# Optimization experiments

Measured on AMD Instinct MI355X. Metric: run time of the kernel, lower is better.

## Reference

```python
import jax, jax.numpy as jnp
import numpy as np

NUM_QUANTIZERS = 8  # num_quantizes in __init__


def l2norm(t, eps=1e-12):
    return t / jnp.clip(jnp.linalg.norm(t, axis=-1, keepdims=True), eps)


def setup_inputs() -> dict:
    key = jax.random.key(0)
    k1, k2 = jax.random.split(key)
    x = jax.random.normal(k1, (1, 16384, 512), dtype=jnp.float32)
    codebook = jax.random.normal(k2, (2048, 512), dtype=jnp.float32)
    return {"x": x, "codebook": codebook}


def reference(x, codebook):
    # cosine-sim codebook: codes live on the unit sphere
    cb = l2norm(codebook)  # [K, D]

    def step(residual, _):
        rn = l2norm(residual)                       # [1, S, D]
        sim = jnp.einsum('bsd,kd->bsk', rn, cb)     # [1, S, K]
        idx = jnp.argmax(sim, axis=-1)              # [1, S]
        q = cb[idx]                                 # [1, S, D] gather
        # commit loss: mse(quantize.detach(), input)
        commit = jnp.mean((jax.lax.stop_gradient(q) - residual) ** 2)
        # straight-through estimator
        q_st = residual + jax.lax.stop_gradient(q - residual)
        return residual - q_st, (q_st, idx, commit)

    _, (quantized, indices, commits) = jax.lax.scan(
        step, x, None, length=NUM_QUANTIZERS)
    # quantized: [n, 1, S, D]; sum over quantizer axis (keepdim batch=1)
    quantized_sum = jnp.sum(quantized, axis=0)      # [1, S, D]
    all_indices = jnp.transpose(indices, (1, 2, 0))  # [1, S, n]
    commit_losses = commits[None, :]                # [1, n]
    return quantized_sum, all_indices, commit_losses
```

## Files before the change

### kernel.cpp

```cpp
#include <hip/hip_runtime.h>
#include <math.h>


#define TOKENS 16384
#define DDIM   512
#define NCODE  2048
#define NQ     8
#define CHUNK  4096
#define DTHR   1e-3f

typedef short   bf16x8  __attribute__((ext_vector_type(8)));
typedef float   f32x4   __attribute__((ext_vector_type(4)));
typedef short   s16x8   __attribute__((ext_vector_type(8)));

#define GLOBAL_AS __attribute__((address_space(1)))
#define LDS_AS    __attribute__((address_space(3)))

#define CBN_OFF  0u
#define G_OFF    1048576u
#define S_OFF    5242880u
#define XHI_OFF  13631488u
#define XLO_OFF  17825792u
#define BHI_OFF  22020096u
#define BLO_OFF  22544384u
#define ACC_OFF  23068672u

#define QS_OFF   0u
#define IDX_OFF  8388608u
#define CL_OFF   8519680u

__device__ inline unsigned short f2bf(float f) {
  unsigned u = __float_as_uint(f);
  return (unsigned short)((u + 0x7FFFu + ((u >> 16) & 1u)) >> 16);
}
__device__ inline float bf2f(unsigned short h) {
  return __uint_as_float(((unsigned)h) << 16);
}

__global__ __launch_bounds__(256) void normalize_cb(const float* __restrict__ cb,
                                                    float* __restrict__ cbn,
                                                    short* __restrict__ bhi,
                                                    short* __restrict__ blo,
                                                    float* __restrict__ acc) {
  if (blockIdx.x == 0 && threadIdx.x < NQ) acc[threadIdx.x] = 0.0f;
  int lane = threadIdx.x & 63;
  int wv   = threadIdx.x >> 6;
  int row  = blockIdx.x * 4 + wv;
  const float4* rp = (const float4*)(cb + (size_t)row * DDIM);
  float4 a = rp[lane * 2 + 0];
  float4 b = rp[lane * 2 + 1];
  float ss = a.x*a.x + a.y*a.y + a.z*a.z + a.w*a.w
           + b.x*b.x + b.y*b.y + b.z*b.z + b.w*b.w;
  #pragma unroll
  for (int o = 1; o < 64; o <<= 1) ss += __shfl_xor(ss, o);
  float nrm = fmaxf(sqrtf(ss), 1e-12f);
  float v[8] = {a.x/nrm, a.y/nrm, a.z/nrm, a.w/nrm,
                b.x/nrm, b.y/nrm, b.z/nrm, b.w/nrm};
  float4* op = (float4*)(cbn + (size_t)row * DDIM);
  op[lane*2+0] = make_float4(v[0], v[1], v[2], v[3]);
  op[lane*2+1] = make_float4(v[4], v[5], v[6], v[7]);

  s16x8 h8, l8;
  #pragma unroll
  for (int i = 0; i < 8; ++i) {
    unsigned short h = f2bf(v[i]);
    h8[i] = (short)h;
    l8[i] = (short)f2bf(v[i] - bf2f(h));
  }
  int nb = row >> 7, rr = row & 127, ks = lane >> 2, g = lane & 3;
  size_t gidx = ((size_t)((nb * 16 + ks) * 4 + g) * 128 + rr) * 8;
  *(s16x8*)(bhi + gidx) = h8;
  *(s16x8*)(blo + gidx) = l8;
}

__global__ __launch_bounds__(256) void split_x(const float* __restrict__ x,
                                               short* __restrict__ xhi,
                                               short* __restrict__ xlo) {
  int gid = blockIdx.x * 256 + threadIdx.x;
  int r  = gid & 127;
  int g  = (gid >> 7) & 3;
  int ks = (gid >> 9) & 15;
  int mb = gid >> 13;
  const float4* src = (const float4*)(x + (size_t)(mb * 128 + r) * DDIM + ks * 32 + g * 8);
  float4 v0 = src[0], v1 = src[1];
  float v[8] = {v0.x, v0.y, v0.z, v0.w, v1.x, v1.y, v1.z, v1.w};
  s16x8 h8, l8;
  #pragma unroll
  for (int i = 0; i < 8; ++i) {
    unsigned short h = f2bf(v[i]);
    h8[i] = (short)h;
    l8[i] = (short)f2bf(v[i] - bf2f(h));
  }
  *(s16x8*)(xhi + (size_t)gid * 8) = h8;
  *(s16x8*)(xlo + (size_t)gid * 8) = l8;
}

__global__ void finalize(const float* __restrict__ acc, float* __restrict__ out) {
  if (threadIdx.x < NQ)
    out[CL_OFF + threadIdx.x] = acc[threadIdx.x] * (1.0f / ((float)TOKENS * (float)DDIM));
}

__global__ __launch_bounds__(256) void gemm_nt(const float* __restrict__ A,
                                               const float* __restrict__ B,
                                               float* __restrict__ C) {
  const int K = DDIM, N = NCODE;
  __shared__ float As[2][16][132];
  __shared__ float Bs[2][16][132];
  const int bn = blockIdx.x * 128;
  const int bm = blockIdx.y * 128;
  const int t  = threadIdx.x;
  const int tx = t & 15;
  const int ty = t >> 4;
  const int lr = t >> 2;
  const int lc = (t & 3) * 4;

  float acc[8][8];
  #pragma unroll
  for (int i = 0; i < 8; ++i)
    #pragma unroll
    for (int j = 0; j < 8; ++j) acc[i][j] = 0.0f;

  const float* Ap = A + (size_t)(bm + lr) * K + lc;
  const float* Bp = B + (size_t)(bn + lr) * K + lc;

  float4 a0 = *(const float4*)(Ap);
  float4 a1 = *(const float4*)(Ap + (size_t)64 * K);
  float4 b0 = *(const float4*)(Bp);
  float4 b1 = *(const float4*)(Bp + (size_t)64 * K);

  int cur = 0;
  for (int k0 = 0; k0 < K; k0 += 16) {
    As[cur][lc+0][lr]    = a0.x; As[cur][lc+1][lr]    = a0.y;
    As[cur][lc+2][lr]    = a0.z; As[cur][lc+3][lr]    = a0.w;
    As[cur][lc+0][lr+64] = a1.x; As[cur][lc+1][lr+64] = a1.y;
    As[cur][lc+2][lr+64] = a1.z; As[cur][lc+3][lr+64] = a1.w;
    Bs[cur][lc+0][lr]    = b0.x; Bs[cur][lc+1][lr]    = b0.y;
    Bs[cur][lc+2][lr]    = b0.z; Bs[cur][lc+3][lr]    = b0.w;
    Bs[cur][lc+0][lr+64] = b1.x; Bs[cur][lc+1][lr+64] = b1.y;
    Bs[cur][lc+2][lr+64] = b1.z; Bs[cur][lc+3][lr+64] = b1.w;
    if (k0 + 16 < K) {
      a0 = *(const float4*)(Ap + k0 + 16);
      a1 = *(const float4*)(Ap + (size_t)64 * K + k0 + 16);
      b0 = *(const float4*)(Bp + k0 + 16);
      b1 = *(const float4*)(Bp + (size_t)64 * K + k0 + 16);
    }
    __syncthreads();
    #pragma unroll
    for (int kk = 0; kk < 16; ++kk) {
      float av[8], bv[8];
      *(float4*)(av + 0) = *(const float4*)&As[cur][kk][ty * 4];
      *(float4*)(av + 4) = *(const float4*)&As[cur][kk][ty * 4 + 64];
      *(float4*)(bv + 0) = *(const float4*)&Bs[cur][kk][tx * 4];
      *(float4*)(bv + 4) = *(const float4*)&Bs[cur][kk][tx * 4 + 64];
      #pragma unroll
      for (int i = 0; i < 8; ++i)
        #pragma unroll
        for (int j = 0; j < 8; ++j) acc[i][j] += av[i] * bv[j];
    }
    cur ^= 1;
  }

  #pragma unroll
  for (int i = 0; i < 8; ++i) {
    int m = bm + ty * 4 + (i & 3) + ((i >> 2) << 6);
    float4 v0 = make_float4(acc[i][0], acc[i][1], acc[i][2], acc[i][3]);
    float4 v1 = make_float4(acc[i][4], acc[i][5], acc[i][6], acc[i][7]);
    *(float4*)&C[(size_t)m * N + bn + tx * 4]      = v0;
    *(float4*)&C[(size_t)m * N + bn + tx * 4 + 64] = v1;
  }
}

__global__ __launch_bounds__(256) void mfma_s(const short* __restrict__ xhi,
                                              const short* __restrict__ xlo,
                                              const short* __restrict__ bhi,
                                              const short* __restrict__ blo,
                                              float* __restrict__ S, int mb0) {
  __shared__ short lds[2][4][4096];
  const int l  = threadIdx.x & 63;
  const int w  = threadIdx.x >> 6;
  const int wm = w >> 1, wn = w & 1;
  const int MB = mb0 + blockIdx.y;
  const int NB = blockIdx.x;

  const short* src = (w == 0) ? xhi : (w == 1) ? xlo : (w == 2) ? bhi : blo;
  const size_t tb  = (size_t)(((w < 2 ? MB : NB) * 16)) * 4096;

  f32x4 acc[4][4];
  #pragma unroll
  for (int i = 0; i < 4; ++i)
    #pragma unroll
    for (int j = 0; j < 4; ++j)
      acc[i][j] = (f32x4){0.f, 0.f, 0.f, 0.f};

  #define STAGE(buf, ks)                                                        \
    {                                                                           \
      const short* gsrc = src + tb + (size_t)(ks) * 4096 + l * 8;               \
      short* ldst = &lds[buf][w][0];                                            \
      _Pragma("unroll")                                                         \
      for (int c = 0; c < 8; ++c)                                               \
        __builtin_amdgcn_global_load_lds(                                       \
            (GLOBAL_AS const unsigned int*)(gsrc + c * 512),                    \
            (LDS_AS unsigned int*)(ldst + c * 512), 16, 0, 0);                  \
    }

  STAGE(0, 0);
  const int g = l >> 4, c16 = l & 15;
  for (int ks = 0; ks < 16; ++ks) {
    const int cur = ks & 1;
    __syncthreads();
    if (ks < 15) STAGE(cur ^ 1, ks + 1);
    bf16x8 ah[4], al[4], bh[4], bl[4];
    #pragma unroll
    for (int f = 0; f < 4; ++f) {
      int ar = (g * 128 + (wm * 64 + f * 16 + c16)) * 8;
      int br = (g * 128 + (wn * 64 + f * 16 + c16)) * 8;
      ah[f] = *(const bf16x8*)&lds[cur][0][ar];
      al[f] = *(const bf16x8*)&lds[cur][1][ar];
      bh[f] = *(const bf16x8*)&lds[cur][2][br];
      bl[f] = *(const bf16x8*)&lds[cur][3][br];
    }
    #pragma unroll
    for (int fm = 0; fm < 4; ++fm)
      #pragma unroll
      for (int fn = 0; fn < 4; ++fn) {
        acc[fm][fn] = __builtin_amdgcn_mfma_f32_16x16x32_bf16(ah[fm], bh[fn], acc[fm][fn], 0, 0, 0);
        acc[fm][fn] = __builtin_amdgcn_mfma_f32_16x16x32_bf16(ah[fm], bl[fn], acc[fm][fn], 0, 0, 0);
        acc[fm][fn] = __builtin_amdgcn_mfma_f32_16x16x32_bf16(al[fm], bh[fn], acc[fm][fn], 0, 0, 0);
      }
  }
  #undef STAGE

  #pragma unroll
  for (int fm = 0; fm < 4; ++fm)
    #pragma unroll
    for (int fn = 0; fn < 4; ++fn)
      #pragma unroll
      for (int reg = 0; reg < 4; ++reg) {
        int m = blockIdx.y * 128 + wm * 64 + fm * 16 + g * 4 + reg;
        int n = NB * 128 + wn * 64 + fn * 16 + c16;
        S[(size_t)m * NCODE + n] = acc[fm][fn][reg];
      }
}

__global__ __launch_bounds__(256) void vq_steps(const float* __restrict__ S,
                                                const float* __restrict__ G,
                                                const float* __restrict__ cbn,
                                                const float* __restrict__ x,
                                                float* __restrict__ out,
                                                float* __restrict__ acc,
                                                int tok0) {
  const int lane = threadIdx.x & 63;
  const int wv   = threadIdx.x >> 6;
  const int trel = blockIdx.x * 4 + wv;
  const int tok  = tok0 + trel;

  float s[32];
  const float4* sp = (const float4*)(S + (size_t)trel * NCODE);
  #pragma unroll
  for (int q = 0; q < 8; ++q) {
    float4 v = sp[q * 64 + lane];
    s[q*4+0] = v.x; s[q*4+1] = v.y; s[q*4+2] = v.z; s[q*4+3] = v.w;
  }

  const float4* xp = (const float4*)(x + (size_t)tok * DDIM);
  float4 x0 = xp[lane * 2 + 0];
  float4 x1 = xp[lane * 2 + 1];
  float rho = x0.x*x0.x + x0.y*x0.y + x0.z*x0.z + x0.w*x0.w
            + x1.x*x1.x + x1.y*x1.y + x1.z*x1.z + x1.w*x1.w;
  #pragma unroll
  for (int o = 1; o < 64; o <<= 1) rho += __shfl_xor(rho, o);

  float qs[8] = {0.f,0.f,0.f,0.f,0.f,0.f,0.f,0.f};
  __shared__ float cl[4][NQ];
  int i0=0,i1=0,i2=0,i3=0,i4=0,i5=0,i6=0;

  for (int t = 0; t < NQ; ++t) {
    float tv[16]; int tc[16];
    #pragma unroll
    for (int r = 0; r < 16; ++r) {
      int ca = ((2*r) >> 2 << 8) + lane * 4 + ((2*r) & 3);
      float va = s[2*r], vb = s[2*r+1];
      bool b = vb > va;
      tv[r] = b ? vb : va;
      tc[r] = b ? ca + 1 : ca;
    }
    #pragma unroll
    for (int h = 8; h >= 1; h >>= 1) {
      #pragma unroll
      for (int r = 0; r < 16; ++r) {
        if (r < h) {
          bool b = tv[r + h] > tv[r];
          tv[r] = b ? tv[r + h] : tv[r];
          tc[r] = b ? tc[r + h] : tc[r];
        }
      }
    }
    float mv = tv[0];
    int   mc = tc[0];
    #pragma unroll
    for (int o = 1; o < 64; o <<= 1) {
      float ov = __shfl_xor(mv, o);
      int   oc = __shfl_xor(mc, o);
      if (ov > mv || (ov == mv && oc < mc)) { mv = ov; mc = oc; }
    }

    int cloc = 0;
    #pragma unroll
    for (int r = 0; r < 32; ++r) cloc += (s[r] >= mv - DTHR) ? 1 : 0;
    #pragma unroll
    for (int o = 1; o < 64; o <<= 1) cloc += __shfl_xor(cloc, o);
    if (cloc > 1) {
      float bv = -3.4e38f; int bc = 0x7FFFFFFF; int seen = 0;
      for (int r = 0; r < 32 && seen < 64; ++r) {
        unsigned long long mask = __ballot(s[r] >= mv - DTHR);
        while (mask && seen < 64) {
          int L = __ffsll((unsigned long long)mask) - 1;
          mask &= mask - 1;
          int kc = ((r >> 2) << 8) + L * 4 + (r & 3);
          if (lane == seen) {
            float e = 0.f;
            const float* xr = x + (size_t)tok * DDIM;
            const float* cr = cbn + (size_t)kc * DDIM;
            for (int k = 0; k < DDIM; ++k) e = fmaf(xr[k], cr[k], e);
            if (t > 0) e -= G[(size_t)i0 * NCODE + kc];
            if (t > 1) e -= G[(size_t)i1 * NCODE + kc];
            if (t > 2) e -= G[(size_t)i2 * NCODE + kc];
            if (t > 3) e -= G[(size_t)i3 * NCODE + kc];
            if (t > 4) e -= G[(size_t)i4 * NCODE + kc];
            if (t > 5) e -= G[(size_t)i5 * NCODE + kc];
            if (t > 6) e -= G[(size_t)i6 * NCODE + kc];
            bv = e; bc = kc;
          }
          ++seen;
        }
      }
      #pragma unroll
      for (int o = 1; o < 64; o <<= 1) {
        float ov = __shfl_xor(bv, o);
        int   oc = __shfl_xor(bc, o);
        if (ov > bv || (ov == bv && oc < bc)) { bv = ov; bc = oc; }
      }
      mv = bv; mc = bc;
    }

    if (t == 0) i0 = mc; else if (t == 1) i1 = mc; else if (t == 2) i2 = mc;
    else if (t == 3) i3 = mc; else if (t == 4) i4 = mc; else if (t == 5) i5 = mc;
    else if (t == 6) i6 = mc;

    rho = rho - 2.0f * mv + 1.0f;
    if (lane == 0) {
      cl[wv][t] = rho;
      out[IDX_OFF + (size_t)tok * NQ + t] = (float)mc;
    }

    const float4* cr = (const float4*)(cbn + (size_t)mc * DDIM);
    float4 c0 = cr[lane * 2 + 0];
    float4 c1 = cr[lane * 2 + 1];
    qs[0]+=c0.x; qs[1]+=c0.y; qs[2]+=c0.z; qs[3]+=c0.w;
    qs[4]+=c1.x; qs[5]+=c1.y; qs[6]+=c1.z; qs[7]+=c1.w;

    if (t < NQ - 1) {
      const float4* gr = (const float4*)(G + (size_t)mc * NCODE);
      #pragma unroll
      for (int q = 0; q < 8; ++q) {
        float4 gv = gr[q * 64 + lane];
        s[q*4+0] -= gv.x; s[q*4+1] -= gv.y; s[q*4+2] -= gv.z; s[q*4+3] -= gv.w;
      }
    }
  }

  float4* op = (float4*)(out + QS_OFF + (size_t)tok * DDIM);
  op[lane * 2 + 0] = make_float4(qs[0], qs[1], qs[2], qs[3]);
  op[lane * 2 + 1] = make_float4(qs[4], qs[5], qs[6], qs[7]);

  __syncthreads();
  if (threadIdx.x < NQ) {
    float v = cl[0][threadIdx.x] + cl[1][threadIdx.x]
            + cl[2][threadIdx.x] + cl[3][threadIdx.x];
    atomicAdd(&acc[threadIdx.x], v);
  }
}

extern "C" void kernel_launch(void* const* d_in, const int* in_sizes, int n_in,
                              void* d_out, int out_size, void* d_ws, size_t ws_size,
                              hipStream_t stream) {
  const float* x  = (const float*)d_in[0];
  const float* cb = (const float*)d_in[1];
  float* out = (float*)d_out;
  float* ws  = (float*)d_ws;

  float* cbn = ws + CBN_OFF;
  float* G   = ws + G_OFF;
  float* S   = ws + S_OFF;
  short* xhi = (short*)(ws + XHI_OFF);
  short* xlo = (short*)(ws + XLO_OFF);
  short* bhi = (short*)(ws + BHI_OFF);
  short* blo = (short*)(ws + BLO_OFF);
  float* acc = ws + ACC_OFF;

  normalize_cb<<<NCODE / 4, 256, 0, stream>>>(cb, cbn, bhi, blo, acc);
  split_x<<<4096, 256, 0, stream>>>(x, xhi, xlo);
  gemm_nt<<<dim3(NCODE / 128, NCODE / 128), 256, 0, stream>>>(cbn, cbn, G);

  for (int c = 0; c < TOKENS / CHUNK; ++c) {
    mfma_s<<<dim3(NCODE / 128, CHUNK / 128), 256, 0, stream>>>(
        xhi, xlo, bhi, blo, S, c * (CHUNK / 128));
    vq_steps<<<CHUNK / 4, 256, 0, stream>>>(S, G, cbn, x, out, acc, c * CHUNK);
  }

  finalize<<<1, 64, 0, stream>>>(acc, out);
}
```

Before: 668.9 us.

## Simplify argmax to value-max plus ballot, move quantized sum to separate kernel

The per-step argmax now tracks only the maximum value with an fmax tree and a shuffle reduction. The winning index is recovered with a ballot over the near-tie mask, falling back to the exact recompute path only when several candidates fall within the threshold. The codebook-row accumulation for the quantized sum moves out of vq_steps into a new qsum kernel that reads the stored indices, and vq_steps gets a higher occupancy hint in launch_bounds. This is meant to cut register pressure and instruction count in the latency-bound step loop, at the cost of an extra kernel launch and re-reading the indices and codebook rows.

```diff
diff --git a/kernel.cpp b/kernel.cpp
--- a/kernel.cpp
+++ b/kernel.cpp
@@ -242,13 +242,13 @@
       }
 }
 
-__global__ __launch_bounds__(256) void vq_steps(const float* __restrict__ S,
-                                                const float* __restrict__ G,
-                                                const float* __restrict__ cbn,
-                                                const float* __restrict__ x,
-                                                float* __restrict__ out,
-                                                float* __restrict__ acc,
-                                                int tok0) {
+__global__ __launch_bounds__(256, 8) void vq_steps(const float* __restrict__ S,
+                                                   const float* __restrict__ G,
+                                                   const float* __restrict__ cbn,
+                                                   const float* __restrict__ x,
+                                                   float* __restrict__ out,
+                                                   float* __restrict__ acc,
+                                                   int tok0) {
   const int lane = threadIdx.x & 63;
   const int wv   = threadIdx.x >> 6;
   const int trel = blockIdx.x * 4 + wv;
@@ -270,51 +270,42 @@
   #pragma unroll
   for (int o = 1; o < 64; o <<= 1) rho += __shfl_xor(rho, o);
 
-  float qs[8] = {0.f,0.f,0.f,0.f,0.f,0.f,0.f,0.f};
   __shared__ float cl[4][NQ];
   int i0=0,i1=0,i2=0,i3=0,i4=0,i5=0,i6=0;
 
   for (int t = 0; t < NQ; ++t) {
-    float tv[16]; int tc[16];
-    #pragma unroll
-    for (int r = 0; r < 16; ++r) {
-      int ca = ((2*r) >> 2 << 8) + lane * 4 + ((2*r) & 3);
-      float va = s[2*r], vb = s[2*r+1];
-      bool b = vb > va;
-      tv[r] = b ? vb : va;
-      tc[r] = b ? ca + 1 : ca;
-    }
-    #pragma unroll
-    for (int h = 8; h >= 1; h >>= 1) {
-      #pragma unroll
-      for (int r = 0; r < 16; ++r) {
-        if (r < h) {
-          bool b = tv[r + h] > tv[r];
-          tv[r] = b ? tv[r + h] : tv[r];
-          tc[r] = b ? tc[r + h] : tc[r];
-        }
-      }
-    }
-    float mv = tv[0];
-    int   mc = tc[0];
-    #pragma unroll
-    for (int o = 1; o < 64; o <<= 1) {
-      float ov = __shfl_xor(mv, o);
-      int   oc = __shfl_xor(mc, o);
-      if (ov > mv || (ov == mv && oc < mc)) { mv = ov; mc = oc; }
-    }
-
-    int cloc = 0;
-    #pragma unroll
-    for (int r = 0; r < 32; ++r) cloc += (s[r] >= mv - DTHR) ? 1 : 0;
-    #pragma unroll
-    for (int o = 1; o < 64; o <<= 1) cloc += __shfl_xor(cloc, o);
-    if (cloc > 1) {
+    float u[11];
+    #pragma unroll
+    for (int i = 0; i < 10; ++i)
+      u[i] = fmaxf(fmaxf(s[3*i], s[3*i+1]), s[3*i+2]);
+    u[10] = fmaxf(s[30], s[31]);
+    float w0 = fmaxf(fmaxf(u[0], u[1]), u[2]);
+    float w1 = fmaxf(fmaxf(u[3], u[4]), u[5]);
+    float w2 = fmaxf(fmaxf(u[6], u[7]), u[8]);
+    float w3 = fmaxf(u[9], u[10]);
+    float m  = fmaxf(fmaxf(fmaxf(w0, w1), w2), w3);
+    #pragma unroll
+    for (int o = 1; o < 64; o <<= 1) m = fmaxf(m, __shfl_xor(m, o));
+
+    const float thr = m - DTHR;
+    unsigned cmask = 0u;
+    #pragma unroll
+    for (int r = 0; r < 32; ++r) cmask |= (s[r] >= thr) ? (1u << r) : 0u;
+    unsigned long long b1 = __ballot(cmask != 0u);
+    unsigned long long b2 = __ballot(__popc(cmask) > 1);
+
+    float mv = m;
+    int   mc;
+    if (__popcll(b1) == 1 && b2 == 0ull) {
+      int r  = __ffs(cmask) - 1;
+      int ca = ((r >> 2) << 8) + lane * 4 + (r & 3);
+      mc = __shfl(ca, (int)(__ffsll(b1) - 1));
+    } else {
       float bv = -3.4e38f; int bc = 0x7FFFFFFF; int seen = 0;
       for (int r = 0; r < 32 && seen < 64; ++r) {
-        unsigned long long mask = __ballot(s[r] >= mv - DTHR);
+        unsigned long long mask = __ballot(s[r] >= thr);
         while (mask && seen < 64) {
-          int L = __ffsll((unsigned long long)mask) - 1;
+          int L = __ffsll(mask) - 1;
           mask &= mask - 1;
           int kc = ((r >> 2) << 8) + L * 4 + (r & 3);
           if (lane == seen) {
@@ -342,6 +333,7 @@
       }
       mv = bv; mc = bc;
     }
+    mc = __builtin_amdgcn_readfirstlane(mc);
 
     if (t == 0) i0 = mc; else if (t == 1) i1 = mc; else if (t == 2) i2 = mc;
     else if (t == 3) i3 = mc; else if (t == 4) i4 = mc; else if (t == 5) i5 = mc;
@@ -352,12 +344,6 @@
       cl[wv][t] = rho;
       out[IDX_OFF + (size_t)tok * NQ + t] = (float)mc;
     }
-
-    const float4* cr = (const float4*)(cbn + (size_t)mc * DDIM);
-    float4 c0 = cr[lane * 2 + 0];
-    float4 c1 = cr[lane * 2 + 1];
-    qs[0]+=c0.x; qs[1]+=c0.y; qs[2]+=c0.z; qs[3]+=c0.w;
-    qs[4]+=c1.x; qs[5]+=c1.y; qs[6]+=c1.z; qs[7]+=c1.w;
 
     if (t < NQ - 1) {
       const float4* gr = (const float4*)(G + (size_t)mc * NCODE);
@@ -369,16 +355,36 @@
     }
   }
 
-  float4* op = (float4*)(out + QS_OFF + (size_t)tok * DDIM);
-  op[lane * 2 + 0] = make_float4(qs[0], qs[1], qs[2], qs[3]);
-  op[lane * 2 + 1] = make_float4(qs[4], qs[5], qs[6], qs[7]);
-
   __syncthreads();
   if (threadIdx.x < NQ) {
     float v = cl[0][threadIdx.x] + cl[1][threadIdx.x]
             + cl[2][threadIdx.x] + cl[3][threadIdx.x];
     atomicAdd(&acc[threadIdx.x], v);
   }
+}
+
+__global__ __launch_bounds__(256) void qsum(const float* __restrict__ cbn,
+                                            float* __restrict__ out) {
+  const int lane = threadIdx.x & 63;
+  const int wv   = threadIdx.x >> 6;
+  const int tok  = blockIdx.x * 4 + wv;
+
+  float idxf = 0.f;
+  if (lane < NQ) idxf = out[IDX_OFF + (size_t)tok * NQ + lane];
+
+  float qs[8] = {0.f,0.f,0.f,0.f,0.f,0.f,0.f,0.f};
+  #pragma unroll
+  for (int t = 0; t < NQ; ++t) {
+    int id = (int)__shfl(idxf, t);
+    const float4* cr = (const float4*)(cbn + (size_t)id * DDIM);
+    float4 c0 = cr[lane * 2 + 0];
+    float4 c1 = cr[lane * 2 + 1];
+    qs[0]+=c0.x; qs[1]+=c0.y; qs[2]+=c0.z; qs[3]+=c0.w;
+    qs[4]+=c1.x; qs[5]+=c1.y; qs[6]+=c1.z; qs[7]+=c1.w;
+  }
+  float4* op = (float4*)(out + QS_OFF + (size_t)tok * DDIM);
+  op[lane * 2 + 0] = make_float4(qs[0], qs[1], qs[2], qs[3]);
+  op[lane * 2 + 1] = make_float4(qs[4], qs[5], qs[6], qs[7]);
 }
 
 extern "C" void kernel_launch(void* const* d_in, const int* in_sizes, int n_in,
@@ -408,5 +414,6 @@
     vq_steps<<<CHUNK / 4, 256, 0, stream>>>(S, G, cbn, x, out, acc, c * CHUNK);
   }
 
+  qsum<<<TOKENS / 4, 256, 0, stream>>>(cbn, out);
   finalize<<<1, 64, 0, stream>>>(acc, out);
 }
```

Result: slower. 820.0 us (+22.6%).
